# Performance work log

Hardware: AMD Instinct MI355X
Metric: run time of the kernel (lower is better)

## Reference

```python
import jax, jax.numpy as jnp
import numpy as np

B, S, DIM = 2, 2048, 2048
H = 16
Q_LORA, KV_LORA = 768, 512
NOPE, ROPE, VD = 128, 64, 128
QKD = NOPE + ROPE  # 192
SOFTCAP = 30.0
EPS = 1e-6
NEG = -1e9
SCALE = QKD ** -0.5  # max_seq_len <= original_seq_len -> no mscale correction


def rms_norm(x, w, eps=EPS):
    xf = x.astype(jnp.float32)
    y = xf * jax.lax.rsqrt(jnp.mean(xf * xf, axis=-1, keepdims=True) + eps)
    return (y * w.astype(jnp.float32)).astype(x.dtype)


def apply_rope(x, cos, sin):
    # x: [B, S, H, D] with interleaved (even, odd) pairs; cos/sin: [S, D//2]
    xr = x.astype(jnp.float32).reshape(*x.shape[:-1], -1, 2)
    xe, xo = xr[..., 0], xr[..., 1]
    c = cos[None, :, None, :]
    s = sin[None, :, None, :]
    ye = xe * c - xo * s
    yo = xe * s + xo * c
    return jnp.stack([ye, yo], axis=-1).reshape(x.shape).astype(x.dtype)


def setup_inputs():
    key = jax.random.key(0)
    ks = jax.random.split(key, 6)
    def w(k, shape, fan_in):
        return jax.random.normal(k, shape, jnp.float32) * (fan_in ** -0.5)
    x = jax.random.normal(ks[0], (B, S, DIM), jnp.float32)
    wq_a_w = w(ks[1], (Q_LORA, DIM), DIM)
    wq_b_w = w(ks[2], (H * QKD, Q_LORA), Q_LORA)
    wkv_a_w = w(ks[3], (KV_LORA + ROPE, DIM), DIM)
    wkv_b_w = w(ks[4], (H * (NOPE + VD), KV_LORA), KV_LORA)
    wo_w = w(ks[5], (DIM, H * VD), H * VD)
    q_norm_w = jnp.ones((Q_LORA,), jnp.float32)
    kv_norm_w = jnp.ones((KV_LORA,), jnp.float32)
    q_gain = jnp.full((H,), 1.5, jnp.float32)  # qk_gain_init
    inv_freq = 1.0 / (10000.0 ** (np.arange(0, ROPE, 2, dtype=np.float32) / ROPE))
    fr = np.outer(np.arange(S, dtype=np.float32), inv_freq)  # [S, 32]
    freqs_cos = jnp.asarray(np.cos(fr))
    freqs_sin = jnp.asarray(np.sin(fr))
    mask = jnp.asarray(np.where(np.triu(np.ones((S, S), dtype=bool), 1), NEG, 0.0).astype(np.float32))
    return dict(x=x, wq_a_w=wq_a_w, q_norm_w=q_norm_w, wq_b_w=wq_b_w, q_gain=q_gain,
                wkv_a_w=wkv_a_w, kv_norm_w=kv_norm_w, wkv_b_w=wkv_b_w, wo_w=wo_w,
                freqs_cos=freqs_cos, freqs_sin=freqs_sin, mask=mask, start_pos=0)


def reference(x, wq_a_w, q_norm_w, wq_b_w, q_gain, wkv_a_w, kv_norm_w, wkv_b_w, wo_w,
              freqs_cos, freqs_sin, mask, start_pos):
    b, s, _ = x.shape
    # low-rank Q: wq_a -> RMSNorm -> wq_b
    q = rms_norm(x @ wq_a_w.T, q_norm_w) @ wq_b_w.T          # [B,S,H*QKD]
    q = q.reshape(b, s, H, QKD)
    q_nope, q_pe = q[..., :NOPE], q[..., NOPE:]
    q_pe = apply_rope(q_pe, freqs_cos, freqs_sin)            # rope_dims=0 -> full 64-dim rotation
    q_pe = q_pe * q_gain[None, None, :, None]                # learned per-head QK gain
    # low-rank KV + decoupled rope key
    kv_full = x @ wkv_a_w.T                                  # [B,S,KV_LORA+ROPE]
    kv, k_pe = kv_full[..., :KV_LORA], kv_full[..., KV_LORA:]
    kv = rms_norm(kv, kv_norm_w)
    k_pe = apply_rope(k_pe[:, :, None, :], freqs_cos, freqs_sin)  # [B,S,1,ROPE]
    # prefill (mask is not None) branch: expand latent kv through wkv_b
    kvb = (kv @ wkv_b_w.T).reshape(b, s, H, NOPE + VD)
    k_nope, v = kvb[..., :NOPE], kvb[..., NOPE:]
    k = jnp.concatenate([k_nope, jnp.broadcast_to(k_pe, (b, s, H, ROPE))], axis=-1)
    qf = jnp.concatenate([q_nope, q_pe], axis=-1)            # [B,S,H,QKD]
    scores = jnp.einsum('bshd,bthd->bsht', qf, k) * SCALE
    scores = SOFTCAP * jnp.tanh(scores / SOFTCAP)            # logit softcap
    scores = scores + mask[None, :, None, :]                 # causal additive mask [S,T]
    p = jax.nn.softmax(scores.astype(jnp.float32), axis=-1).astype(x.dtype)
    y = jnp.einsum('bsht,bthd->bshd', p, v)                  # [B,S,H,VD]
    # XSA: subtract self-value projection
    vn = v * jax.lax.rsqrt(jnp.maximum(jnp.sum(v * v, axis=-1, keepdims=True), 1e-12))
    y = y - jnp.sum(y * vn, axis=-1, keepdims=True) * vn
    return y.reshape(b, s, H * VD) @ wo_w.T                  # [B,S,DIM]
```

## Files before the change

### kernel.cpp

```cpp
#include <hip/hip_runtime.h>
#include <stdint.h>

typedef unsigned short u16;
typedef __bf16 bf16x8 __attribute__((ext_vector_type(8)));
typedef float f32x4 __attribute__((ext_vector_type(4)));
typedef unsigned int u32x4 __attribute__((ext_vector_type(4)));
typedef unsigned int u32x2 __attribute__((ext_vector_type(2)));

typedef __attribute__((address_space(3))) void LDSV;
typedef __attribute__((address_space(1))) void GLV;

#define S_LEN 2048

__device__ __forceinline__ float bf2f(u16 u) {
  union { unsigned int i; float f; } v; v.i = ((unsigned int)u) << 16; return v.f;
}
__device__ __forceinline__ u16 f2bf(float f) {
  union { float f; unsigned int i; } v; v.f = f;
  unsigned int x = v.i;
  return (u16)((x + 0x7fffu + ((x >> 16) & 1u)) >> 16);
}
__device__ __forceinline__ unsigned int cvtpk(float lo, float hi) {
  unsigned int r;
  asm("v_cvt_pk_bf16_f32 %0, %1, %2" : "=v"(r) : "v"(lo), "v"(hi));
  return r;
}
__device__ __forceinline__ unsigned long long pack4(float4 v) {
  return (unsigned long long)f2bf(v.x)
       | ((unsigned long long)f2bf(v.y) << 16)
       | ((unsigned long long)f2bf(v.z) << 32)
       | ((unsigned long long)f2bf(v.w) << 48);
}

__global__ __launch_bounds__(256) void cast_all(
    const float* __restrict__ s0, u16* __restrict__ d0, long e0,
    const float* __restrict__ s1, u16* __restrict__ d1, long e1,
    const float* __restrict__ s2, u16* __restrict__ d2, long e2,
    const float* __restrict__ s3, u16* __restrict__ d3, long e3,
    const float* __restrict__ s4, u16* __restrict__ d4, long e4,
    const float* __restrict__ s5, u16* __restrict__ d5, long e5) {
  long i = (long)blockIdx.x * 256 + threadIdx.x;
  const float* src; u16* dst; long base; bool pad = false;
  if (i < e0)      { src = s0; dst = d0; base = 0; }
  else if (i < e1) { src = s1; dst = d1; base = e0; }
  else if (i < e2) { src = s2; dst = d2; base = e1; }
  else if (i < e3) { src = s3; dst = d3; base = e2; }
  else if (i < e4) { src = s4; dst = d4; base = e3; }
  else if (i < e5) { src = s5; dst = d5; base = e4; pad = true; }
  else return;
  long li = i - base;
  long elem0 = li * 4;
  unsigned long long r = 0;
  if (!pad || (elem0 >> 11) < 576)
    r = pack4(*(const float4*)(src + elem0));
  ((unsigned long long*)dst)[li] = r;
}

template <int MODE>
__global__ __launch_bounds__(256) void gemm_nt(const u16* __restrict__ A, int lda,
                                               const u16* __restrict__ B, int ldb,
                                               void* __restrict__ Cv, int ldc,
                                               u16* __restrict__ Vc, int K) {
  __shared__ u16 As[128 * 64];
  __shared__ u16 Bs[128 * 64];
  const int tid = threadIdx.x;
  const int lane = tid & 63, wid = tid >> 6;
  const int l15 = lane & 15, l4 = lane >> 4;
  const int wr = wid >> 1, wc = wid & 1;
  const long bm = (long)blockIdx.y * 128;
  const long bn = (long)blockIdx.x * 128;

  const int srow = wid * 32 + (lane >> 3);
  const int scol = (lane & 7) * 8;
  const u16* Ag = A + (bm + srow) * (long)lda + scol;
  const u16* Bg = B + (bn + srow) * (long)ldb + scol;
  u16* AsW = &As[wid * 32 * 64];
  u16* BsW = &Bs[wid * 32 * 64];

  f32x4 acc[4][4] = {};

  for (int k0 = 0; k0 < K; k0 += 64) {
    __syncthreads();
#pragma unroll
    for (int ch = 0; ch < 4; ++ch) {
      __builtin_amdgcn_global_load_lds((const GLV*)(Ag + (long)ch * 8 * lda + k0),
                                       (LDSV*)(AsW + ch * 512), 16, 0, 0);
      __builtin_amdgcn_global_load_lds((const GLV*)(Bg + (long)ch * 8 * ldb + k0),
                                       (LDSV*)(BsW + ch * 512), 16, 0, 0);
    }
    __syncthreads();
#pragma unroll
    for (int kk = 0; kk < 2; ++kk) {
      bf16x8 af[4], bfr[4];
#pragma unroll
      for (int m = 0; m < 4; ++m)
        af[m] = *(const bf16x8*)(&As[(wr * 64 + m * 16 + l15) * 64 + (kk * 4 + l4) * 8]);
#pragma unroll
      for (int n = 0; n < 4; ++n)
        bfr[n] = *(const bf16x8*)(&Bs[(wc * 64 + n * 16 + l15) * 64 + (kk * 4 + l4) * 8]);
#pragma unroll
      for (int m = 0; m < 4; ++m)
#pragma unroll
        for (int n = 0; n < 4; ++n)
          acc[m][n] = __builtin_amdgcn_mfma_f32_16x16x32_bf16(af[m], bfr[n], acc[m][n], 0, 0, 0);
    }
  }
#pragma unroll
  for (int m = 0; m < 4; ++m)
#pragma unroll
    for (int n = 0; n < 4; ++n)
#pragma unroll
      for (int r = 0; r < 4; ++r) {
        long row = bm + wr * 64 + m * 16 + l4 * 4 + r;
        long col = bn + wc * 64 + n * 16 + l15;
        float v = acc[m][n][r];
        if constexpr (MODE == 0) {
          ((u16*)Cv)[row * ldc + col] = f2bf(v);
        } else if constexpr (MODE == 1) {
          ((float*)Cv)[row * ldc + col] = v;
        } else {
          int h = (int)(col >> 8), c = (int)(col & 255);
          if (c < 128)
            ((u16*)Cv)[(((row >> 11) * 16 + h) * 2048 + (row & 2047)) * 128 + c] = f2bf(v);
          else
            Vc[row * 2048 + h * 128 + (c - 128)] = f2bf(v);
        }
      }
}

__global__ __launch_bounds__(256) void rmsnorm2_kernel(u16* __restrict__ qakv,
                                                       const float* __restrict__ qw,
                                                       const float* __restrict__ kvw) {
  __shared__ float sred[4];
  const int tid = threadIdx.x;
  const int row = blockIdx.x;
  if (row < 4096) {
    u16* p = qakv + (size_t)row * 1408;
    float x[3];
    float ss = 0.f;
#pragma unroll
    for (int i = 0; i < 3; ++i) { x[i] = bf2f(p[tid + i * 256]); ss += x[i] * x[i]; }
#pragma unroll
    for (int off = 1; off < 64; off <<= 1) ss += __shfl_xor(ss, off);
    if ((tid & 63) == 0) sred[tid >> 6] = ss;
    __syncthreads();
    float tot = sred[0] + sred[1] + sred[2] + sred[3];
    float rs = rsqrtf(tot * (1.0f / 768.0f) + 1e-6f) * 0.0069411711f;
#pragma unroll
    for (int i = 0; i < 3; ++i) p[tid + i * 256] = f2bf(x[i] * rs * qw[tid + i * 256]);
  } else {
    u16* p = qakv + (size_t)(row - 4096) * 1408 + 768;
    float x[2];
    float ss = 0.f;
#pragma unroll
    for (int i = 0; i < 2; ++i) { x[i] = bf2f(p[tid + i * 256]); ss += x[i] * x[i]; }
#pragma unroll
    for (int off = 1; off < 64; off <<= 1) ss += __shfl_xor(ss, off);
    if ((tid & 63) == 0) sred[tid >> 6] = ss;
    __syncthreads();
    float tot = sred[0] + sred[1] + sred[2] + sred[3];
    float rs = rsqrtf(tot * (1.0f / 512.0f) + 1e-6f);
#pragma unroll
    for (int i = 0; i < 2; ++i) p[tid + i * 256] = f2bf(x[i] * rs * kvw[tid + i * 256]);
  }
}

__global__ __launch_bounds__(256) void rope_q_kernel(u16* __restrict__ q,
                                                     const float* __restrict__ cosb,
                                                     const float* __restrict__ sinb,
                                                     const float* __restrict__ gain) {
  int idx = blockIdx.x * 256 + threadIdx.x;
  int i = idx & 31;
  int h = (idx >> 5) & 15;
  int srow = idx >> 9;
  int s = srow & (S_LEN - 1);
  size_t base = (size_t)srow * 3072 + h * 192 + 128 + 2 * i;
  unsigned int* p = (unsigned int*)(q + base);
  unsigned int v = *p;
  float xe = bf2f((u16)(v & 0xffff)), xo = bf2f((u16)(v >> 16));
  float c = cosb[s * 32 + i], sn = sinb[s * 32 + i];
  float g = gain[h];
  float ye = (xe * c - xo * sn) * g, yo = (xe * sn + xo * c) * g;
  *p = (unsigned int)f2bf(ye) | ((unsigned int)f2bf(yo) << 16);
}

__global__ __launch_bounds__(256) void ropek_kernel(const u16* __restrict__ qakv,
                                                    const float* __restrict__ cosb,
                                                    const float* __restrict__ sinb,
                                                    u16* __restrict__ kpe) {
  int idx = blockIdx.x * 256 + threadIdx.x;
  int i = idx & 31;
  int srow = idx >> 5;
  int s = srow & 2047;
  unsigned int v = *(const unsigned int*)(qakv + (size_t)srow * 1408 + 1280 + 2 * i);
  float xe = bf2f((u16)(v & 0xffff)), xo = bf2f((u16)(v >> 16));
  float c = cosb[s * 32 + i], sn = sinb[s * 32 + i];
  *(unsigned int*)(kpe + (size_t)srow * 64 + 2 * i) =
      (unsigned int)f2bf(xe * c - xo * sn) | ((unsigned int)f2bf(xe * sn + xo * c) << 16);
}

__global__ __launch_bounds__(256) void v_transpose_kernel(const u16* __restrict__ Vc,
                                                          u16* __restrict__ VT) {
  __shared__ u16 tile[64][65];
  int bh = blockIdx.z;
  int d0 = blockIdx.y * 64;
  int t0 = blockIdx.x * 64;
  int b = bh >> 4, h = bh & 15;
#pragma unroll
  for (int i = 0; i < 2; ++i) {
    int flat = i * 256 + threadIdx.x;
    int t = flat >> 3, c = (flat & 7) * 8;
    u32x4 v = *(const u32x4*)(Vc + ((long)b * S_LEN + t0 + t) * 2048 + h * 128 + d0 + c);
    const u16* pv = (const u16*)&v;
#pragma unroll
    for (int j = 0; j < 8; ++j) tile[c + j][t] = pv[j];
  }
  __syncthreads();
#pragma unroll
  for (int i = 0; i < 2; ++i) {
    int flat = i * 256 + threadIdx.x;
    int d = flat >> 3, tc = (flat & 7) * 8;
    u32x4 v;
    u16* pv = (u16*)&v;
#pragma unroll
    for (int j = 0; j < 8; ++j) pv[j] = tile[d][tc + j];
    *(u32x4*)(VT + ((long)bh * 128 + d0 + d) * S_LEN + t0 + tc) = v;
  }
}

__global__ __launch_bounds__(512, 2) void attn_kernel(const u16* __restrict__ Qg,
                                                      const u16* __restrict__ KbN,
                                                      const u16* __restrict__ Kpe,
                                                      const u16* __restrict__ VTg,
                                                      const u16* __restrict__ Vcg,
                                                      u16* __restrict__ Yg) {
  __shared__ u16 Ks[64 * 192];
  __shared__ u16 VTs[128 * 64];
  __shared__ u16 Ps[128 * 64];

  const int tid = threadIdx.x, lane = tid & 63, wid = tid >> 6;
  const int l15 = lane & 15, l4 = lane >> 4;

  const int p = blockIdx.x;
  const int bh = (p & 7) * 4 + (p >> 6);
  const int pair = (p >> 3) & 7;
  const int b = bh >> 4, h = bh & 15;

  const u16* Kn = KbN + (long)bh * S_LEN * 128;
  const u16* Kp = Kpe + (long)b * S_LEN * 64;
  const u16* Vbh = VTg + (long)bh * 128 * S_LEN;

  int krow[3], sst[3];
  const u16* sb[3];
  u16* ksw[3];
#pragma unroll
  for (int i = 0; i < 3; ++i) {
    int flat = i * 512 + tid;
    int r = flat / 24, c = flat % 24;
    krow[i] = r;
    if (c < 16) { sb[i] = Kn + c * 8; sst[i] = 128; }
    else        { sb[i] = Kp + (c - 16) * 8; sst[i] = 64; }
    ksw[i] = &Ks[r * 192 + ((c ^ (r & 7)) * 8)];
  }
  int vrow[2], vc[2];
  u16* vsw[2];
#pragma unroll
  for (int i = 0; i < 2; ++i) {
    int flat = i * 512 + tid;
    vrow[i] = flat >> 3; vc[i] = flat & 7;
    vsw[i] = &VTs[vrow[i] * 64 + ((vc[i] ^ (vrow[i] & 7)) * 8)];
  }

  const int prow = wid * 16 + l15;
  const int pr7 = prow & 7;

  for (int seg = 0; seg < 2; ++seg) {
    const int qt = seg ? pair : 15 - pair;
    const int q0 = qt * 128;
    const int nkt = 2 * qt + 2;

    bf16x8 qf[6];
    {
      const u16* qb_ = Qg + ((long)b * S_LEN + q0 + prow) * 3072 + h * 192;
#pragma unroll
      for (int f = 0; f < 6; ++f) qf[f] = *(const bf16x8*)(qb_ + f * 32 + 8 * l4);
    }

    f32x4 o[8] = {};
    float lsum = 0.f;

    u32x4 ka[3], va[2];
#pragma unroll
    for (int i = 0; i < 3; ++i)
      ka[i] = *(const u32x4*)(sb[i] + (long)krow[i] * sst[i]);
#pragma unroll
    for (int i = 0; i < 2; ++i)
      va[i] = *(const u32x4*)(Vbh + (long)vrow[i] * S_LEN + vc[i] * 8);

    for (int it = 0; it < nkt; ++it) {
      __syncthreads();
#pragma unroll
      for (int i = 0; i < 3; ++i) *(u32x4*)ksw[i] = ka[i];
#pragma unroll
      for (int i = 0; i < 2; ++i) *(u32x4*)vsw[i] = va[i];
      __syncthreads();
      if (it + 1 < nkt) {
        int k0n = (it + 1) * 64;
#pragma unroll
        for (int i = 0; i < 3; ++i)
          ka[i] = *(const u32x4*)(sb[i] + (long)(k0n + krow[i]) * sst[i]);
#pragma unroll
        for (int i = 0; i < 2; ++i)
          va[i] = *(const u32x4*)(Vbh + (long)vrow[i] * S_LEN + k0n + vc[i] * 8);
      }

      f32x4 sacc[4] = {};
      __builtin_amdgcn_s_setprio(1);
#pragma unroll
      for (int f = 0; f < 6; ++f)
#pragma unroll
        for (int tf = 0; tf < 4; ++tf) {
          int row = tf * 16 + l15;
          bf16x8 kf = *(const bf16x8*)(&Ks[row * 192 + (((f * 4 + l4) ^ (row & 7)) * 8)]);
          sacc[tf] = __builtin_amdgcn_mfma_f32_16x16x32_bf16(kf, qf[f], sacc[tf], 0, 0, 0);
        }
      __builtin_amdgcn_s_setprio(0);

#pragma unroll
      for (int tf = 0; tf < 4; ++tf)
#pragma unroll
        for (int r = 0; r < 4; ++r) {
          float u = __builtin_amdgcn_exp2f(sacc[tf][r]);
          sacc[tf][r] = __builtin_amdgcn_exp2f(-86.56170245333781f *
                                               __builtin_amdgcn_rcpf(u + 1.0f));
        }
      if (it * 64 >= q0) {
        const int dthr = q0 + prow - it * 64 - l4 * 4;
#pragma unroll
        for (int tf = 0; tf < 4; ++tf)
#pragma unroll
          for (int r = 0; r < 4; ++r)
            if (tf * 16 + r > dthr) sacc[tf][r] = 0.f;
      }
#pragma unroll
      for (int tf = 0; tf < 4; ++tf)
#pragma unroll
        for (int r = 0; r < 4; ++r) lsum += sacc[tf][r];

#pragma unroll
      for (int tf = 0; tf < 4; ++tf) {
        u32x2 w;
        w.x = cvtpk(sacc[tf][0], sacc[tf][1]);
        w.y = cvtpk(sacc[tf][2], sacc[tf][3]);
        int chunk = tf * 2 + (l4 >> 1);
        *(u32x2*)(&Ps[prow * 64 + ((chunk ^ pr7) * 8) + (l4 & 1) * 4]) = w;
      }

      __builtin_amdgcn_s_setprio(1);
#pragma unroll
      for (int kk = 0; kk < 2; ++kk) {
        bf16x8 pf = *(const bf16x8*)(&Ps[prow * 64 + (((kk * 4 + l4) ^ pr7) * 8)]);
#pragma unroll
        for (int nf = 0; nf < 8; ++nf) {
          int vr = nf * 16 + l15;
          bf16x8 vf = *(const bf16x8*)(&VTs[vr * 64 + (((kk * 4 + l4) ^ (vr & 7)) * 8)]);
          o[nf] = __builtin_amdgcn_mfma_f32_16x16x32_bf16(pf, vf, o[nf], 0, 0, 0);
        }
      }
      __builtin_amdgcn_s_setprio(0);
    }

    lsum += __shfl_xor(lsum, 16);
    lsum += __shfl_xor(lsum, 32);
    float inv[4];
#pragma unroll
    for (int r = 0; r < 4; ++r)
      inv[r] = __builtin_amdgcn_rcpf(__shfl(lsum, (wid << 6 & 0) + l4 * 4 + r));

    float yv[8][4], vvv[8][4];
    float ssum[4] = {0.f, 0.f, 0.f, 0.f}, dsum[4] = {0.f, 0.f, 0.f, 0.f};
    const u16* vb = Vcg + ((long)b * S_LEN + q0 + wid * 16) * 2048 + h * 128;
#pragma unroll
    for (int nf = 0; nf < 8; ++nf)
#pragma unroll
      for (int r = 0; r < 4; ++r) {
        float vv = bf2f(vb[(l4 * 4 + r) * 2048 + nf * 16 + l15]);
        float y = o[nf][r] * inv[r];
        vvv[nf][r] = vv; yv[nf][r] = y;
        ssum[r] += vv * vv; dsum[r] += y * vv;
      }
#pragma unroll
    for (int r = 0; r < 4; ++r) {
      ssum[r] += __shfl_xor(ssum[r], 1); ssum[r] += __shfl_xor(ssum[r], 2);
      ssum[r] += __shfl_xor(ssum[r], 4); ssum[r] += __shfl_xor(ssum[r], 8);
      dsum[r] += __shfl_xor(dsum[r], 1); dsum[r] += __shfl_xor(dsum[r], 2);
      dsum[r] += __shfl_xor(dsum[r], 4); dsum[r] += __shfl_xor(dsum[r], 8);
      dsum[r] *= __builtin_amdgcn_rcpf(fmaxf(ssum[r], 1e-12f));
    }
#pragma unroll
    for (int nf = 0; nf < 8; ++nf)
#pragma unroll
      for (int r = 0; r < 4; ++r) {
        long row = (long)b * S_LEN + q0 + wid * 16 + l4 * 4 + r;
        Yg[row * 2048 + h * 128 + nf * 16 + l15] = f2bf(yv[nf][r] - dsum[r] * vvv[nf][r]);
      }
  }
}

extern "C" void kernel_launch(void* const* d_in, const int* in_sizes, int n_in,
                              void* d_out, int out_size, void* d_ws, size_t ws_size,
                              hipStream_t stream) {
  const float* x       = (const float*)d_in[0];
  const float* wq_a    = (const float*)d_in[1];
  const float* q_norm  = (const float*)d_in[2];
  const float* wq_b    = (const float*)d_in[3];
  const float* q_gain  = (const float*)d_in[4];
  const float* wkv_a   = (const float*)d_in[5];
  const float* kv_norm = (const float*)d_in[6];
  const float* wkv_b   = (const float*)d_in[7];
  const float* wo      = (const float*)d_in[8];
  const float* fcos    = (const float*)d_in[9];
  const float* fsin    = (const float*)d_in[10];
  float* out = (float*)d_out;

  char* ws = (char*)d_ws;
  size_t off = 0;
  auto alloc = [&](size_t bytes) {
    char* pp = ws + off;
    off += (bytes + 255) & ~(size_t)255;
    return pp;
  };
  const long M = 4096;
  u16* xb    = (u16*)alloc(M * 2048 * 2);
  u16* wcomb = (u16*)alloc(1408L * 2048 * 2);
  u16* wqbb  = (u16*)alloc(3072L * 768 * 2);
  u16* wkvbb = (u16*)alloc(4096L * 512 * 2);
  u16* wob   = (u16*)alloc(2048L * 2048 * 2);
  u16* qakv  = (u16*)alloc(M * 1408 * 2);
  u16* qb    = (u16*)alloc(M * 3072 * 2);
  u16* KbN   = (u16*)alloc(32L * 2048 * 128 * 2);
  u16* kpe   = (u16*)alloc(M * 64 * 2);
  u16* Vc    = (u16*)alloc(M * 2048 * 2);
  u16* VTb   = (u16*)alloc(32L * 128 * 2048 * 2);
  u16* Yb    = (u16*)alloc(M * 2048 * 2);

  const long n4_x = 2097152, n4_wqa = 393216, n4_wqb = 589824,
             n4_wkvb = 524288, n4_wo = 1048576, n4_wkvap = 327680;
  long e0 = n4_x, e1 = e0 + n4_wqa, e2 = e1 + n4_wqb, e3 = e2 + n4_wkvb,
       e4 = e3 + n4_wo, e5 = e4 + n4_wkvap;
  cast_all<<<(int)(e5 / 256), 256, 0, stream>>>(
      x, xb, e0, wq_a, wcomb, e1, wq_b, wqbb, e2, wkv_b, wkvbb, e3,
      wo, wob, e4, wkv_a, wcomb + 768L * 2048, e5);

  gemm_nt<0><<<dim3(11, 32), 256, 0, stream>>>(xb, 2048, wcomb, 2048, qakv, 1408, nullptr, 2048);
  rmsnorm2_kernel<<<8192, 256, 0, stream>>>(qakv, q_norm, kv_norm);
  gemm_nt<0><<<dim3(24, 32), 256, 0, stream>>>(qakv, 1408, wqbb, 768, qb, 3072, nullptr, 768);
  rope_q_kernel<<<2097152 / 256, 256, 0, stream>>>(qb, fcos, fsin, q_gain);
  ropek_kernel<<<131072 / 256, 256, 0, stream>>>(qakv, fcos, fsin, kpe);
  gemm_nt<2><<<dim3(32, 32), 256, 0, stream>>>(qakv + 768, 1408, wkvbb, 512, KbN, 0, Vc, 512);
  v_transpose_kernel<<<dim3(32, 2, 32), 256, 0, stream>>>(Vc, VTb);
  attn_kernel<<<256, 512, 0, stream>>>(qb, KbN, kpe, VTb, Vc, Yb);
  gemm_nt<1><<<dim3(16, 32), 256, 0, stream>>>(Yb, 2048, wob, 2048, out, 2048, nullptr, 2048);
}
```

Baseline: 286.0 us.

## Add 256x256-tile 8-wave GEMM with phased LDS pipelining for three projections

```diff
diff --git a/kernel.cpp b/kernel.cpp
--- a/kernel.cpp
+++ b/kernel.cpp
@@ -128,6 +128,150 @@
       }
 }
 
+#define MM_PHASE(QM, QN, BB)                                                     \
+  __builtin_amdgcn_s_setprio(1);                                                 \
+  {                                                                              \
+    _Pragma("unroll") for (int mf = 0; mf < 4; ++mf) {                           \
+      _Pragma("unroll") for (int nf = 0; nf < 2; ++nf) {                         \
+        _Pragma("unroll") for (int kk = 0; kk < 2; ++kk) {                       \
+          acc[(QM) * 4 + mf][(QN) * 2 + nf] =                                    \
+              __builtin_amdgcn_mfma_f32_16x16x32_bf16(                           \
+                  a[mf][kk], BB[nf][kk], acc[(QM) * 4 + mf][(QN) * 2 + nf],      \
+                  0, 0, 0);                                                      \
+        }                                                                        \
+      }                                                                          \
+    }                                                                            \
+  }                                                                              \
+  __builtin_amdgcn_s_setprio(0);
+
+template <int MODE>
+__global__ __launch_bounds__(512, 2) void gemm256(const u16* __restrict__ A, int lda,
+                                                  const u16* __restrict__ B, int ldb,
+                                                  void* __restrict__ Cv, int ldc,
+                                                  u16* __restrict__ Vc, int K) {
+  __shared__ u16 SMEM[65536];
+  const int tid = threadIdx.x;
+  const int lane = tid & 63, wid = tid >> 6;
+  const int l15 = lane & 15, l4 = lane >> 4;
+  const int wm16 = (wid >> 2) * 16, wn16 = (wid & 3) * 16;
+
+  const int gx = gridDim.x, nwg = gx * gridDim.y;
+  int lin0 = blockIdx.y * gx + blockIdx.x;
+  int cpx = nwg >> 3;
+  int swzb = (lin0 & 7) * cpx + (lin0 >> 3);
+  const long bm = (long)(swzb / gx) * 256;
+  const long bn = (long)(swzb % gx) * 256;
+
+  long aoff[2], boff[2];
+#pragma unroll
+  for (int j = 0; j < 2; ++j) {
+    int lb = (j * 512 + tid) * 16;
+    int swz = lb ^ (((lb >> 7) & 7) << 4);
+    int sr = swz >> 7, sc = (swz & 127) >> 1;
+    aoff[j] = (bm + sr) * (long)lda + sc;
+    boff[j] = (bn + sr) * (long)ldb + sc;
+  }
+
+  auto STAGE = [&](int buf, int half, int isB, int tt) {
+#pragma unroll
+    for (int j = 0; j < 2; ++j) {
+      const u16* src = isB ? (B + boff[j] + (long)half * 128 * ldb + tt * 64)
+                           : (A + aoff[j] + (long)half * 128 * lda + tt * 64);
+      __builtin_amdgcn_global_load_lds(
+          (const GLV*)src,
+          (LDSV*)((char*)SMEM + isB * 65536 + buf * 32768 + half * 16384 +
+                  (j * 512 + tid) * 16),
+          16, 0, 0);
+    }
+  };
+
+  f32x4 acc[8][4] = {};
+  bf16x8 a[4][2], b0[2][2], b1[2][2];
+
+  auto LDA_ = [&](int buf, int qm) {
+#pragma unroll
+    for (int mf = 0; mf < 4; ++mf)
+#pragma unroll
+      for (int kk = 0; kk < 2; ++kk) {
+        int r = mf * 32 + wm16 + l15;
+        int lb = r * 128 + kk * 64 + l4 * 16;
+        a[mf][kk] = *(const bf16x8*)((char*)SMEM + buf * 32768 + qm * 16384 +
+                                     (lb ^ ((r & 7) << 4)));
+      }
+  };
+  auto LDB_ = [&](int buf, int qn, bf16x8 (*bb)[2]) {
+#pragma unroll
+    for (int nf = 0; nf < 2; ++nf)
+#pragma unroll
+      for (int kk = 0; kk < 2; ++kk) {
+        int r = nf * 64 + wn16 + l15;
+        int lb = r * 128 + kk * 64 + l4 * 16;
+        bb[nf][kk] = *(const bf16x8*)((char*)SMEM + 65536 + buf * 32768 +
+                                      qn * 16384 + (lb ^ ((r & 7) << 4)));
+      }
+  };
+
+  const int NT = K >> 6;
+  STAGE(0, 0, 0, 0); STAGE(0, 0, 1, 0); STAGE(0, 1, 1, 0); STAGE(0, 1, 0, 0);
+  STAGE(1, 0, 0, 1); STAGE(1, 0, 1, 1);
+  asm volatile("s_waitcnt vmcnt(4)" ::: "memory");
+  __builtin_amdgcn_s_barrier();
+
+  for (int t = 0; t < NT; ++t) {
+    const int cb = t & 1;
+    if (t + 1 < NT) STAGE(cb ^ 1, 1, 1, t + 1);
+    LDA_(cb, 0);
+    LDB_(cb, 0, b0);
+    __builtin_amdgcn_s_barrier();
+    asm volatile("s_waitcnt lgkmcnt(0)" ::: "memory");
+    __builtin_amdgcn_sched_barrier(0);
+    MM_PHASE(0, 0, b0);
+    __builtin_amdgcn_s_barrier();
+    if (t + 1 < NT) STAGE(cb ^ 1, 1, 0, t + 1);
+    LDB_(cb, 1, b1);
+    __builtin_amdgcn_s_barrier();
+    asm volatile("s_waitcnt lgkmcnt(0)" ::: "memory");
+    __builtin_amdgcn_sched_barrier(0);
+    MM_PHASE(0, 1, b1);
+    __builtin_amdgcn_s_barrier();
+    if (t + 2 < NT) STAGE(cb, 0, 0, t + 2);
+    LDA_(cb, 1);
+    __builtin_amdgcn_s_barrier();
+    asm volatile("s_waitcnt lgkmcnt(0)" ::: "memory");
+    __builtin_amdgcn_sched_barrier(0);
+    MM_PHASE(1, 0, b0);
+    __builtin_amdgcn_s_barrier();
+    if (t + 2 < NT) STAGE(cb, 0, 1, t + 2);
+    __builtin_amdgcn_s_barrier();
+    MM_PHASE(1, 1, b1);
+    if (t + 2 < NT) asm volatile("s_waitcnt vmcnt(4)" ::: "memory");
+    else            asm volatile("s_waitcnt vmcnt(0)" ::: "memory");
+    __builtin_amdgcn_s_barrier();
+  }
+
+#pragma unroll
+  for (int mfg = 0; mfg < 8; ++mfg)
+#pragma unroll
+    for (int nfg = 0; nfg < 4; ++nfg)
+#pragma unroll
+      for (int r = 0; r < 4; ++r) {
+        long row = bm + mfg * 32 + wm16 + l4 * 4 + r;
+        long col = bn + nfg * 64 + wn16 + l15;
+        float v = acc[mfg][nfg][r];
+        if constexpr (MODE == 0) {
+          ((u16*)Cv)[row * ldc + col] = f2bf(v);
+        } else if constexpr (MODE == 1) {
+          ((float*)Cv)[row * ldc + col] = v;
+        } else {
+          int h = (int)(col >> 8), c = (int)(col & 255);
+          if (c < 128)
+            ((u16*)Cv)[(((row >> 11) * 16 + h) * 2048 + (row & 2047)) * 128 + c] = f2bf(v);
+          else
+            Vc[row * 2048 + h * 128 + (c - 128)] = f2bf(v);
+        }
+      }
+}
+
 __global__ __launch_bounds__(256) void rmsnorm2_kernel(u16* __restrict__ qakv,
                                                        const float* __restrict__ qw,
                                                        const float* __restrict__ kvw) {
@@ -454,11 +598,11 @@
 
   gemm_nt<0><<<dim3(11, 32), 256, 0, stream>>>(xb, 2048, wcomb, 2048, qakv, 1408, nullptr, 2048);
   rmsnorm2_kernel<<<8192, 256, 0, stream>>>(qakv, q_norm, kv_norm);
-  gemm_nt<0><<<dim3(24, 32), 256, 0, stream>>>(qakv, 1408, wqbb, 768, qb, 3072, nullptr, 768);
+  gemm256<0><<<dim3(12, 16), 512, 0, stream>>>(qakv, 1408, wqbb, 768, qb, 3072, nullptr, 768);
   rope_q_kernel<<<2097152 / 256, 256, 0, stream>>>(qb, fcos, fsin, q_gain);
   ropek_kernel<<<131072 / 256, 256, 0, stream>>>(qakv, fcos, fsin, kpe);
-  gemm_nt<2><<<dim3(32, 32), 256, 0, stream>>>(qakv + 768, 1408, wkvbb, 512, KbN, 0, Vc, 512);
+  gemm256<2><<<dim3(16, 16), 512, 0, stream>>>(qakv + 768, 1408, wkvbb, 512, KbN, 0, Vc, 512);
   v_transpose_kernel<<<dim3(32, 2, 32), 256, 0, stream>>>(Vc, VTb);
   attn_kernel<<<256, 512, 0, stream>>>(qb, KbN, kpe, VTb, Vc, Yb);
-  gemm_nt<1><<<dim3(16, 32), 256, 0, stream>>>(Yb, 2048, wob, 2048, out, 2048, nullptr, 2048);
-}
+  gemm256<1><<<dim3(8, 16), 512, 0, stream>>>(Yb, 2048, wob, 2048, out, 2048, nullptr, 2048);
+}
```

After: 276.7 us. 3.3% less time.
